# Kernel tuning notes

Hardware: AMD Instinct MI355X
Metric: run time of the kernel (lower is better)

## Reference

```python
import jax, jax.numpy as jnp
import numpy as np

DIM = 1024
HEADS = 16
SCALE = DIM ** (-0.5)  # note: full dim, matching original module


def setup_inputs() -> dict:
    key = jax.random.key(0)
    k1, k2, k3, k4 = jax.random.split(key, 4)
    x = jax.random.normal(k1, (8, 1024, DIM), dtype=jnp.float32)
    w_qkv = jax.random.normal(k2, (DIM, 3 * DIM), dtype=jnp.float32) * (DIM ** -0.5)
    w_out = jax.random.normal(k3, (DIM, DIM), dtype=jnp.float32) * (DIM ** -0.5)
    b_out = jax.random.normal(k4, (DIM,), dtype=jnp.float32) * 0.01
    return {"x": x, "w_qkv": w_qkv, "w_out": w_out, "b_out": b_out}


def reference(x, w_qkv, w_out, b_out):
    b, n, dim = x.shape
    h = HEADS
    d = dim // h
    qkv = x @ w_qkv  # [b, n, 3*dim]
    q, k, v = jnp.split(qkv, 3, axis=-1)
    # 'b n (h d) -> b h n d'
    def to_heads(t):
        return t.reshape(b, n, h, d).transpose(0, 2, 1, 3)
    q, k, v = to_heads(q), to_heads(k), to_heads(v)
    dots = jnp.einsum('bhid,bhjd->bhij', q, k) * SCALE
    attn = jax.nn.softmax(dots, axis=-1)
    out = jnp.einsum('bhij,bhjd->bhid', attn, v)
    out = out.transpose(0, 2, 1, 3).reshape(b, n, dim)  # 'b h n d -> b n (h d)'
    return out @ w_out + b_out  # dropout is identity (rate=0 / eval)
```

## Files before the change

### kernel.cpp

```cpp
#include <hip/hip_runtime.h>

typedef __bf16 bf16x8 __attribute__((ext_vector_type(8)));
typedef __bf16 bf16x4 __attribute__((ext_vector_type(4)));
typedef float  f32x4  __attribute__((ext_vector_type(4)));

#define MFMA16(a, b, c) __builtin_amdgcn_mfma_f32_16x16x32_bf16(a, b, c, 0, 0, 0)
#define GLL(gp, lp) __builtin_amdgcn_global_load_lds( \
    (__attribute__((address_space(1))) void*)(gp),    \
    (__attribute__((address_space(3))) void*)(lp), 16, 0, 0)
#define WAITBAR(N) asm volatile("s_waitcnt vmcnt(" #N ") lgkmcnt(0)\n\ts_barrier" ::: "memory")

__global__ __launch_bounds__(256) void cast_x_kernel(const float* __restrict__ in,
                                                     __bf16* __restrict__ out) {
  int i = blockIdx.x * 256 + threadIdx.x;
  const float4 v = ((const float4*)in)[i];
  bf16x4 o = {(__bf16)v.x, (__bf16)v.y, (__bf16)v.z, (__bf16)v.w};
  ((bf16x4*)out)[i] = o;
}

__global__ void transpose_cast_kernel(const float* __restrict__ in,
                                      __bf16* __restrict__ out,
                                      int rows, int cols) {
  __shared__ float tile[32][33];
  int tx = threadIdx.x, ty = threadIdx.y;
  int x = blockIdx.x * 32 + tx;
  int y0 = blockIdx.y * 32;
#pragma unroll
  for (int i = 0; i < 32; i += 8)
    tile[ty + i][tx] = in[(y0 + ty + i) * cols + x];
  __syncthreads();
  int ox = y0 + tx;
  int oy0 = blockIdx.x * 32;
#pragma unroll
  for (int i = 0; i < 32; i += 8)
    out[(oy0 + ty + i) * rows + ox] = (__bf16)tile[tx][ty + i];
}

#define QSCALE 0.045084220027780106f
__global__ __launch_bounds__(256) void gemm_bt_kernel(
    const __bf16* __restrict__ A, const __bf16* __restrict__ Bt,
    __bf16* __restrict__ qo, __bf16* __restrict__ ko, __bf16* __restrict__ vo) {
  __shared__ __bf16 LDS[3][2][4096];
  const int tid = threadIdx.x;
  const int id = blockIdx.x;
  const int xcd = id & 7, s = id >> 3;
  const int bx = xcd * 3 + s % 3;
  const int by = s / 3;
  const int m0 = by * 128, n0 = bx * 128;
  const int w = tid >> 6, lane = tid & 63;
  const int quad = lane >> 4, l15 = lane & 15;
  const int wm = (w >> 1) * 64, wn = (w & 1) * 64;
  f32x4 acc[4][4] = {};
  const int sr = tid >> 2;
  const int sc = (tid & 3) * 8;
  const __bf16* ag = A + (m0 + sr) * 1024 + sc;
  const __bf16* bg = Bt + (n0 + sr) * 1024 + sc;

  auto stage = [&](int T, int b) {
    const int kk = T * 32;
    GLL(ag + kk,             &LDS[b][0][0] + w * 512);
    GLL(ag + 64 * 1024 + kk, &LDS[b][0][0] + 2048 + w * 512);
    GLL(bg + kk,             &LDS[b][1][0] + w * 512);
    GLL(bg + 64 * 1024 + kk, &LDS[b][1][0] + 2048 + w * 512);
  };
  auto compute = [&](int b) {
    const __bf16* Asb = &LDS[b][0][0];
    const __bf16* Bsb = &LDS[b][1][0];
    bf16x8 af[4], bfr[4];
#pragma unroll
    for (int i = 0; i < 4; ++i)
      af[i] = *(const bf16x8*)(Asb + (wm + i * 16 + l15) * 32 + quad * 8);
#pragma unroll
    for (int j = 0; j < 4; ++j)
      bfr[j] = *(const bf16x8*)(Bsb + (wn + j * 16 + l15) * 32 + quad * 8);
#pragma unroll
    for (int i = 0; i < 4; ++i)
#pragma unroll
      for (int j = 0; j < 4; ++j)
        acc[i][j] = MFMA16(af[i], bfr[j], acc[i][j]);
  };

  stage(0, 0);
  stage(1, 1);
  WAITBAR(4);
  for (int g = 0; g < 10; ++g) {
    const int t = g * 3;
    stage(t + 2, 2); compute(0); WAITBAR(4);
    stage(t + 3, 0); compute(1); WAITBAR(4);
    stage(t + 4, 1); compute(2); WAITBAR(4);
  }
  compute(0);
  asm volatile("s_waitcnt vmcnt(0) lgkmcnt(0)\n\ts_barrier" ::: "memory");
  compute(1);
  __syncthreads();

  const int gcw = n0 + wn;
  float* T = (float*)(&LDS[0][0][0]) + w * 1088;
  const int which = gcw >> 10;
  const int h = (gcw & 1023) >> 6;
  if (which == 2) {
#pragma unroll
    for (int i = 0; i < 4; ++i) {
      int gm = m0 + wm + i * 16 + quad * 4;
      int b = gm >> 10, n = gm & 1023;
      __bf16* vb = vo + ((long)(b * 16 + h) * 64) * 1024 + n;
#pragma unroll
      for (int j = 0; j < 4; ++j) {
        int dd = j * 16 + l15;
        bf16x4 pv = {(__bf16)acc[i][j][0], (__bf16)acc[i][j][1],
                     (__bf16)acc[i][j][2], (__bf16)acc[i][j][3]};
        *(bf16x4*)(vb + (long)dd * 1024) = pv;
      }
    }
  } else {
    __bf16* dst = (which == 0) ? qo : ko;
    const float scl = (which == 0) ? QSCALE : 1.0f;
#pragma unroll
    for (int i = 0; i < 4; ++i) {
#pragma unroll
      for (int j = 0; j < 4; ++j)
#pragma unroll
        for (int r = 0; r < 4; ++r)
          T[(quad * 4 + r) * 68 + j * 16 + l15] = acc[i][j][r];
      const float* Tr = T + l15 * 68 + quad * 16;
      f32x4 c0 = *(const f32x4*)(Tr);
      f32x4 c1 = *(const f32x4*)(Tr + 4);
      f32x4 c2 = *(const f32x4*)(Tr + 8);
      f32x4 c3 = *(const f32x4*)(Tr + 12);
      int gm = m0 + wm + i * 16 + l15;
      int b = gm >> 10, n = gm & 1023;
      __bf16* p = dst + ((long)((b * 16 + h) * 1024 + n)) * 64 + quad * 16;
      bf16x8 o0 = {(__bf16)(c0[0] * scl), (__bf16)(c0[1] * scl),
                   (__bf16)(c0[2] * scl), (__bf16)(c0[3] * scl),
                   (__bf16)(c1[0] * scl), (__bf16)(c1[1] * scl),
                   (__bf16)(c1[2] * scl), (__bf16)(c1[3] * scl)};
      bf16x8 o1 = {(__bf16)(c2[0] * scl), (__bf16)(c2[1] * scl),
                   (__bf16)(c2[2] * scl), (__bf16)(c2[3] * scl),
                   (__bf16)(c3[0] * scl), (__bf16)(c3[1] * scl),
                   (__bf16)(c3[2] * scl), (__bf16)(c3[3] * scl)};
      *(bf16x8*)p = o0;
      *(bf16x8*)(p + 8) = o1;
    }
  }
}

__global__ __launch_bounds__(256) void gemm_out_kernel(
    const __bf16* __restrict__ A, const __bf16* __restrict__ Bt,
    float* __restrict__ outp, const float* __restrict__ bias) {
  __shared__ __bf16 LDS[3][6144];
  const int tid = threadIdx.x;
  const int id = blockIdx.x;
  const int xcd = id & 7, s = id >> 3;
  const int by = xcd * 8 + (s >> 4);
  const int bx = s & 15;
  const int m0 = by * 128, n0 = bx * 64;
  const int w = tid >> 6, lane = tid & 63;
  const int quad = lane >> 4, l15 = lane & 15;
  const int wm = (w >> 1) * 64, wn = (w & 1) * 32;
  f32x4 acc[4][2] = {};
  const int sr = tid >> 2;
  const int sc = (tid & 3) * 8;
  const __bf16* ag = A + (m0 + sr) * 1024 + sc;
  const __bf16* bg = Bt + (n0 + sr) * 1024 + sc;

  auto stage = [&](int T, int b) {
    const int kk = T * 32;
    GLL(ag + kk,             &LDS[b][0] + w * 512);
    GLL(ag + 64 * 1024 + kk, &LDS[b][0] + 2048 + w * 512);
    GLL(bg + kk,             &LDS[b][0] + 4096 + w * 512);
  };
  auto compute = [&](int b) {
    const __bf16* Asb = &LDS[b][0];
    const __bf16* Bsb = &LDS[b][0] + 4096;
    bf16x8 af[4], bfr[2];
#pragma unroll
    for (int i = 0; i < 4; ++i)
      af[i] = *(const bf16x8*)(Asb + (wm + i * 16 + l15) * 32 + quad * 8);
#pragma unroll
    for (int j = 0; j < 2; ++j)
      bfr[j] = *(const bf16x8*)(Bsb + (wn + j * 16 + l15) * 32 + quad * 8);
#pragma unroll
    for (int i = 0; i < 4; ++i)
#pragma unroll
      for (int j = 0; j < 2; ++j)
        acc[i][j] = MFMA16(af[i], bfr[j], acc[i][j]);
  };

  stage(0, 0);
  stage(1, 1);
  WAITBAR(3);
  for (int g = 0; g < 10; ++g) {
    const int t = g * 3;
    stage(t + 2, 2); compute(0); WAITBAR(3);
    stage(t + 3, 0); compute(1); WAITBAR(3);
    stage(t + 4, 1); compute(2); WAITBAR(3);
  }
  compute(0);
  asm volatile("s_waitcnt vmcnt(0) lgkmcnt(0)\n\ts_barrier" ::: "memory");
  compute(1);
  __syncthreads();

  const int cb = n0 + wn;
  float* T = (float*)(&LDS[0][0]) + w * 592;
  f32x4 bv0 = *(const f32x4*)(bias + cb + quad * 8);
  f32x4 bv1 = *(const f32x4*)(bias + cb + quad * 8 + 4);
#pragma unroll
  for (int i = 0; i < 4; ++i) {
#pragma unroll
    for (int j = 0; j < 2; ++j)
#pragma unroll
      for (int r = 0; r < 4; ++r)
        T[(quad * 4 + r) * 36 + j * 16 + l15] = acc[i][j][r];
    const float* Tr = T + l15 * 36 + quad * 8;
    f32x4 v0 = *(const f32x4*)(Tr);
    f32x4 v1 = *(const f32x4*)(Tr + 4);
    v0 += bv0;
    v1 += bv1;
    int gm = m0 + wm + i * 16 + l15;
    float* p = outp + (long)gm * 1024 + cb + quad * 8;
    *(f32x4*)(p) = v0;
    *(f32x4*)(p + 4) = v1;
  }
}

__global__ __launch_bounds__(256, 4) void attn_kernel(
    const __bf16* __restrict__ q, const __bf16* __restrict__ k,
    const __bf16* __restrict__ vt, __bf16* __restrict__ ao) {
  __shared__ __bf16 KV[2][128 * 64];
  __shared__ __bf16 Ps[4][32 * 32];
  __bf16* const Ks = KV[0];
  __bf16* const Vs = KV[1];
  const int tid = threadIdx.x;
  const int bh = blockIdx.x & 127, qt = blockIdx.x >> 7;
  const int w = tid >> 6, lane = tid & 63;
  const int quad = lane >> 4, l15 = lane & 15;
  const int qrow = qt * 128 + w * 32;
  const __bf16* qb = q + (bh * 1024 + qrow) * 64;
  bf16x8 qf[2][2];
#pragma unroll
  for (int f = 0; f < 2; ++f) {
    qf[f][0] = *(const bf16x8*)(qb + (f * 16 + l15) * 64 + quad * 8);
    qf[f][1] = *(const bf16x8*)(qb + (f * 16 + l15) * 64 + 32 + quad * 8);
  }
  f32x4 o[2][4] = {};
  float rs0 = 0.f, rs1 = 0.f;
  const int krow = tid >> 3, kg8 = tid & 7;
  const __bf16* kg = k + (bh * 1024 + krow) * 64 + kg8 * 8;
  const int ksw = (kg8 ^ (krow & 7)) * 8;
  const int vrow = tid >> 2, vg4 = tid & 3;
  const __bf16* vg = vt + (bh * 64 + vrow) * 1024 + vg4 * 8;
  const int kfs0 = (quad ^ (l15 & 7)) * 8;
  const int kfs1 = ((4 + quad) ^ (l15 & 7)) * 8;
  __bf16* const pw = Ps[w];
  const int psw = quad ^ (l15 & 3);

  bf16x8 kvr[4], vvr[4];
#pragma unroll
  for (int p = 0; p < 4; ++p) kvr[p] = *(const bf16x8*)(kg + (p * 32) * 64);
#pragma unroll
  for (int p = 0; p < 4; ++p) vvr[p] = *(const bf16x8*)(vg + p * 32);

  for (int jt = 0; jt < 8; ++jt) {
    __syncthreads();
#pragma unroll
    for (int p = 0; p < 4; ++p)
      *(bf16x8*)(Ks + (krow + p * 32) * 64 + ksw) = kvr[p];
#pragma unroll
    for (int p = 0; p < 4; ++p)
      *(bf16x8*)(Vs + vrow * 128 + (((p * 4 + vg4) ^ (vrow & 15)) * 8)) = vvr[p];
    __syncthreads();
    if (jt < 7) {
      const int j0n = (jt + 1) * 128;
#pragma unroll
      for (int p = 0; p < 4; ++p) kvr[p] = *(const bf16x8*)(kg + (j0n + p * 32) * 64);
#pragma unroll
      for (int p = 0; p < 4; ++p) vvr[p] = *(const bf16x8*)(vg + j0n + p * 32);
    }
#pragma unroll
    for (int Q = 0; Q < 4; ++Q) {
#pragma unroll
      for (int tl = 0; tl < 2; ++tl) {
        const int t = 2 * Q + tl;
        const __bf16* kr = Ks + (t * 16 + l15) * 64;
        bf16x8 kf0 = *(const bf16x8*)(kr + kfs0);
        bf16x8 kf1 = *(const bf16x8*)(kr + kfs1);
        f32x4 z0 = {}, z1 = {};
        __builtin_amdgcn_s_setprio(1);
        z0 = MFMA16(kf0, qf[0][0], z0);
        z0 = MFMA16(kf1, qf[0][1], z0);
        z1 = MFMA16(kf0, qf[1][0], z1);
        z1 = MFMA16(kf1, qf[1][1], z1);
        __builtin_amdgcn_s_setprio(0);
        const float p00 = __builtin_amdgcn_exp2f(z0[0]), p01 = __builtin_amdgcn_exp2f(z0[1]);
        const float p02 = __builtin_amdgcn_exp2f(z0[2]), p03 = __builtin_amdgcn_exp2f(z0[3]);
        const float p10 = __builtin_amdgcn_exp2f(z1[0]), p11 = __builtin_amdgcn_exp2f(z1[1]);
        const float p12 = __builtin_amdgcn_exp2f(z1[2]), p13 = __builtin_amdgcn_exp2f(z1[3]);
        rs0 += (p00 + p01) + (p02 + p03);
        rs1 += (p10 + p11) + (p12 + p13);
        const int g = (2 * tl + (quad >> 1)) ^ (l15 & 3);
        bf16x4 pa = {(__bf16)p00, (__bf16)p01, (__bf16)p02, (__bf16)p03};
        bf16x4 pb = {(__bf16)p10, (__bf16)p11, (__bf16)p12, (__bf16)p13};
        *(bf16x4*)(pw + l15 * 32 + g * 8 + (quad & 1) * 4) = pa;
        *(bf16x4*)(pw + (16 + l15) * 32 + g * 8 + (quad & 1) * 4) = pb;
      }
      bf16x8 pf0 = *(const bf16x8*)(pw + l15 * 32 + psw * 8);
      bf16x8 pf1 = *(const bf16x8*)(pw + (16 + l15) * 32 + psw * 8);
      __builtin_amdgcn_s_setprio(1);
#pragma unroll
      for (int dt = 0; dt < 4; ++dt) {
        bf16x8 vf = *(const bf16x8*)(Vs + (dt * 16 + l15) * 128 + (((Q * 4 + quad) ^ l15) * 8));
        o[0][dt] = MFMA16(pf0, vf, o[0][dt]);
        o[1][dt] = MFMA16(pf1, vf, o[1][dt]);
      }
      __builtin_amdgcn_s_setprio(0);
    }
  }
  rs0 += __shfl_xor(rs0, 16); rs0 += __shfl_xor(rs0, 32);
  rs1 += __shfl_xor(rs1, 16); rs1 += __shfl_xor(rs1, 32);
  __syncthreads();
  float* const T = (float*)KV + w * 1088;
  const int b = bh >> 4, h = bh & 15;
  const int rr = lane >> 3, c8 = lane & 7;
#pragma unroll
  for (int f = 0; f < 2; ++f) {
    const float rsf = f ? rs1 : rs0;
#pragma unroll
    for (int dt = 0; dt < 4; ++dt)
#pragma unroll
      for (int r = 0; r < 4; ++r)
        T[(quad * 4 + r) * 68 + dt * 16 + l15] = o[f][dt][r];
#pragma unroll
    for (int h2 = 0; h2 < 2; ++h2) {
      const int row = h2 * 8 + rr;
      const float inv = 1.0f / __shfl(rsf, row);
      const float* Tr = T + row * 68 + c8 * 8;
      const f32x4 a0 = *(const f32x4*)(Tr);
      const f32x4 a1 = *(const f32x4*)(Tr + 4);
      bf16x8 ov = {(__bf16)(a0[0] * inv), (__bf16)(a0[1] * inv),
                   (__bf16)(a0[2] * inv), (__bf16)(a0[3] * inv),
                   (__bf16)(a1[0] * inv), (__bf16)(a1[1] * inv),
                   (__bf16)(a1[2] * inv), (__bf16)(a1[3] * inv)};
      const long grow = (long)b * 1024 + qrow + f * 16 + row;
      *(bf16x8*)(ao + grow * 1024 + h * 64 + c8 * 8) = ov;
    }
  }
}

extern "C" void kernel_launch(void* const* d_in, const int* in_sizes, int n_in,
                              void* d_out, int out_size, void* d_ws, size_t ws_size,
                              hipStream_t stream) {
  const float* x = (const float*)d_in[0];
  const float* w_qkv = (const float*)d_in[1];
  const float* w_out = (const float*)d_in[2];
  const float* b_out = (const float*)d_in[3];
  float* out = (float*)d_out;

  char* ws = (char*)d_ws;
  __bf16* xb    = (__bf16*)(ws);
  __bf16* wqkvt = (__bf16*)(ws + 16777216);
  __bf16* woutt = (__bf16*)(ws + 23068672);
  __bf16* qw    = (__bf16*)(ws + 25165824);
  __bf16* kw    = (__bf16*)(ws + 41943040);
  __bf16* vw    = (__bf16*)(ws + 58720256);
  __bf16* ao    = xb;

  cast_x_kernel<<<8192, 256, 0, stream>>>(x, xb);
  transpose_cast_kernel<<<dim3(96, 32), dim3(32, 8), 0, stream>>>(w_qkv, wqkvt, 1024, 3072);
  transpose_cast_kernel<<<dim3(32, 32), dim3(32, 8), 0, stream>>>(w_out, woutt, 1024, 1024);
  gemm_bt_kernel<<<1536, 256, 0, stream>>>(xb, wqkvt, qw, kw, vw);
  attn_kernel<<<1024, 256, 0, stream>>>(qw, kw, vw, ao);
  gemm_out_kernel<<<1024, 256, 0, stream>>>(ao, woutt, out, b_out);
}
```

Baseline: 235.2 us.

## Fuse fp32-to-bf16 cast of x into QKV GEMM and merge weight transposes

Removes the separate x cast kernel: the QKV GEMM now loads fp32 x tiles into registers, converts them to bf16 and writes them to LDS one step ahead, while B still streams through global_load_lds. The two weight transpose-cast launches are merged into one grid. This saves a full write and read of the bf16 copy of x plus two launches. In exchange each of the 1536 GEMM blocks re-reads its A tiles as fp32 (twice the bytes), and the restructured pipeline needs register staging and split wait/barrier points.

```diff
diff --git a/kernel.cpp b/kernel.cpp
--- a/kernel.cpp
+++ b/kernel.cpp
@@ -9,38 +9,40 @@
     (__attribute__((address_space(1))) void*)(gp),    \
     (__attribute__((address_space(3))) void*)(lp), 16, 0, 0)
 #define WAITBAR(N) asm volatile("s_waitcnt vmcnt(" #N ") lgkmcnt(0)\n\ts_barrier" ::: "memory")
-
-__global__ __launch_bounds__(256) void cast_x_kernel(const float* __restrict__ in,
-                                                     __bf16* __restrict__ out) {
-  int i = blockIdx.x * 256 + threadIdx.x;
-  const float4 v = ((const float4*)in)[i];
-  bf16x4 o = {(__bf16)v.x, (__bf16)v.y, (__bf16)v.z, (__bf16)v.w};
-  ((bf16x4*)out)[i] = o;
-}
-
-__global__ void transpose_cast_kernel(const float* __restrict__ in,
-                                      __bf16* __restrict__ out,
-                                      int rows, int cols) {
+#define VWAIT(N)   asm volatile("s_waitcnt vmcnt(" #N ")" ::: "memory")
+#define LBAR()     asm volatile("s_waitcnt lgkmcnt(0)\n\ts_barrier" ::: "memory")
+
+__global__ void transpose_cast2_kernel(const float* __restrict__ in0,
+                                       __bf16* __restrict__ out0,
+                                       const float* __restrict__ in1,
+                                       __bf16* __restrict__ out1) {
   __shared__ float tile[32][33];
+  int bx = blockIdx.x;
+  const float* in;
+  __bf16* out;
+  int rows = 1024, cols;
+  if (bx < 96) { in = in0; out = out0; cols = 3072; }
+  else         { in = in1; out = out1; cols = 1024; bx -= 96; }
   int tx = threadIdx.x, ty = threadIdx.y;
-  int x = blockIdx.x * 32 + tx;
+  int x = bx * 32 + tx;
   int y0 = blockIdx.y * 32;
 #pragma unroll
   for (int i = 0; i < 32; i += 8)
     tile[ty + i][tx] = in[(y0 + ty + i) * cols + x];
   __syncthreads();
   int ox = y0 + tx;
-  int oy0 = blockIdx.x * 32;
+  int oy0 = bx * 32;
 #pragma unroll
   for (int i = 0; i < 32; i += 8)
     out[(oy0 + ty + i) * rows + ox] = (__bf16)tile[tx][ty + i];
 }
 
 #define QSCALE 0.045084220027780106f
-__global__ __launch_bounds__(256) void gemm_bt_kernel(
-    const __bf16* __restrict__ A, const __bf16* __restrict__ Bt,
+__global__ __launch_bounds__(256) void gemm_qkv_kernel(
+    const float* __restrict__ X, const __bf16* __restrict__ Bt,
     __bf16* __restrict__ qo, __bf16* __restrict__ ko, __bf16* __restrict__ vo) {
-  __shared__ __bf16 LDS[3][2][4096];
+  __shared__ __bf16 LA[3 * 4096];
+  __shared__ __bf16 LB[3 * 4096];
   const int tid = threadIdx.x;
   const int id = blockIdx.x;
   const int xcd = id & 7, s = id >> 3;
@@ -53,19 +55,34 @@
   f32x4 acc[4][4] = {};
   const int sr = tid >> 2;
   const int sc = (tid & 3) * 8;
-  const __bf16* ag = A + (m0 + sr) * 1024 + sc;
+  const float*  xg = X + (m0 + sr) * 1024 + sc;
   const __bf16* bg = Bt + (n0 + sr) * 1024 + sc;
 
-  auto stage = [&](int T, int b) {
-    const int kk = T * 32;
-    GLL(ag + kk,             &LDS[b][0][0] + w * 512);
-    GLL(ag + 64 * 1024 + kk, &LDS[b][0][0] + 2048 + w * 512);
-    GLL(bg + kk,             &LDS[b][1][0] + w * 512);
-    GLL(bg + 64 * 1024 + kk, &LDS[b][1][0] + 2048 + w * 512);
-  };
-  auto compute = [&](int b) {
-    const __bf16* Asb = &LDS[b][0][0];
-    const __bf16* Bsb = &LDS[b][1][0];
+  f32x4 ar0[4], ar1[4];
+
+  auto loadA = [&](int T, f32x4* dst) {
+    const float* p = xg + T * 32;
+    dst[0] = *(const f32x4*)(p);
+    dst[1] = *(const f32x4*)(p + 4);
+    dst[2] = *(const f32x4*)(p + 64 * 1024);
+    dst[3] = *(const f32x4*)(p + 64 * 1024 + 4);
+  };
+  auto gllB = [&](int T, int bufo) {
+    const __bf16* gp = bg + T * 32;
+    GLL(gp,             LB + bufo + w * 512);
+    GLL(gp + 64 * 1024, LB + bufo + 2048 + w * 512);
+  };
+  auto dswA = [&](const f32x4* src, int bufo) {
+    bf16x8 v0 = {(__bf16)src[0][0], (__bf16)src[0][1], (__bf16)src[0][2], (__bf16)src[0][3],
+                 (__bf16)src[1][0], (__bf16)src[1][1], (__bf16)src[1][2], (__bf16)src[1][3]};
+    bf16x8 v1 = {(__bf16)src[2][0], (__bf16)src[2][1], (__bf16)src[2][2], (__bf16)src[2][3],
+                 (__bf16)src[3][0], (__bf16)src[3][1], (__bf16)src[3][2], (__bf16)src[3][3]};
+    *(bf16x8*)(LA + bufo + tid * 8) = v0;
+    *(bf16x8*)(LA + bufo + 2048 + tid * 8) = v1;
+  };
+  auto compute = [&](int bufo) {
+    const __bf16* Asb = LA + bufo;
+    const __bf16* Bsb = LB + bufo;
     bf16x8 af[4], bfr[4];
 #pragma unroll
     for (int i = 0; i < 4; ++i)
@@ -80,22 +97,39 @@
         acc[i][j] = MFMA16(af[i], bfr[j], acc[i][j]);
   };
 
-  stage(0, 0);
-  stage(1, 1);
-  WAITBAR(4);
-  for (int g = 0; g < 10; ++g) {
-    const int t = g * 3;
-    stage(t + 2, 2); compute(0); WAITBAR(4);
-    stage(t + 3, 0); compute(1); WAITBAR(4);
-    stage(t + 4, 1); compute(2); WAITBAR(4);
-  }
+  loadA(0, ar0); gllB(0, 0);
+  loadA(1, ar1); gllB(1, 4096);
+  VWAIT(6);
+  dswA(ar0, 0);
+  LBAR();
+
+#define STEP(t, SIN, SOUT)                                            \
+  loadA((t) + 2, SIN); gllB((t) + 2, (((t) + 2) % 3) * 4096);          \
+  VWAIT(6);                                                           \
+  dswA(SOUT, (((t) + 1) % 3) * 4096);                                 \
+  compute(((t) % 3) * 4096);                                          \
+  LBAR();
+
+#pragma unroll 1
+  for (int g = 0; g < 5; ++g) {
+    const int t = g * 6;
+    STEP(t + 0, ar0, ar1)
+    STEP(t + 1, ar1, ar0)
+    STEP(t + 2, ar0, ar1)
+    STEP(t + 3, ar1, ar0)
+    STEP(t + 4, ar0, ar1)
+    STEP(t + 5, ar1, ar0)
+  }
+#undef STEP
+  VWAIT(0);
+  dswA(ar1, 4096);
   compute(0);
-  asm volatile("s_waitcnt vmcnt(0) lgkmcnt(0)\n\ts_barrier" ::: "memory");
-  compute(1);
+  LBAR();
+  compute(4096);
   __syncthreads();
 
   const int gcw = n0 + wn;
-  float* T = (float*)(&LDS[0][0][0]) + w * 1088;
+  float* T = (float*)LA + w * 1088;
   const int which = gcw >> 10;
   const int h = (gcw & 1023) >> 6;
   if (which == 2) {
@@ -356,18 +390,15 @@
   float* out = (float*)d_out;
 
   char* ws = (char*)d_ws;
-  __bf16* xb    = (__bf16*)(ws);
+  __bf16* ao    = (__bf16*)(ws);
   __bf16* wqkvt = (__bf16*)(ws + 16777216);
   __bf16* woutt = (__bf16*)(ws + 23068672);
   __bf16* qw    = (__bf16*)(ws + 25165824);
   __bf16* kw    = (__bf16*)(ws + 41943040);
   __bf16* vw    = (__bf16*)(ws + 58720256);
-  __bf16* ao    = xb;
-
-  cast_x_kernel<<<8192, 256, 0, stream>>>(x, xb);
-  transpose_cast_kernel<<<dim3(96, 32), dim3(32, 8), 0, stream>>>(w_qkv, wqkvt, 1024, 3072);
-  transpose_cast_kernel<<<dim3(32, 32), dim3(32, 8), 0, stream>>>(w_out, woutt, 1024, 1024);
-  gemm_bt_kernel<<<1536, 256, 0, stream>>>(xb, wqkvt, qw, kw, vw);
+
+  transpose_cast2_kernel<<<dim3(128, 32), dim3(32, 8), 0, stream>>>(w_qkv, wqkvt, w_out, woutt);
+  gemm_qkv_kernel<<<1536, 256, 0, stream>>>(x, wqkvt, qw, kw, vw);
   attn_kernel<<<1024, 256, 0, stream>>>(qw, kw, vw, ao);
   gemm_out_kernel<<<1024, 256, 0, stream>>>(ao, woutt, out, b_out);
 }
```

New measurement: 271.4 us. +15.4%, slower.
